# Kernel tuning notes

Measured on AMD Instinct MI355X. Metric: run time of the kernel, lower is better.

## Reference

```python
import jax, jax.numpy as jnp
import numpy as np

B, T, S, H, N = 4, 1024, 1024, 1024, 16
D = H // N
EPS = 1e-12
MASK_FILL = -1e6


def setup_inputs() -> dict:
    key = jax.random.key(0)
    ks = jax.random.split(key, 20)
    w = lambda i: jax.random.normal(ks[i], (H, H), jnp.float32) * 0.02
    zb = jnp.zeros((H,), jnp.float32)
    tgt_mask = jnp.tile(jnp.tril(jnp.ones((T, T), jnp.int32))[None], (B, 1, 1))
    return {
        "encoder_states": jax.random.normal(ks[0], (B, S, H), jnp.float32),
        "decoder_inputs": jax.random.normal(ks[1], (B, T, H), jnp.float32),
        "src_attn_mask": jnp.ones((B, S), jnp.int32),
        "tgt_attn_mask": tgt_mask,
        "q_w": w(2), "q_b": zb,
        "k_w": w(3), "k_b": zb,
        "v_w": w(4), "v_b": zb,
        "sq_w": w(5), "sq_b": zb,
        "sk_w": w(6), "sk_b": zb,
        "sv_w": w(7), "sv_b": zb,
        "dense_w": w(8), "dense_b": zb,
        "ln_g": jnp.ones((H,), jnp.float32),
        "ln_b": zb,
    }


def _layernorm(x, g, b):
    mu = jnp.mean(x, -1, keepdims=True)
    var = jnp.mean(jnp.square(x - mu), -1, keepdims=True)
    return (x - mu) * jax.lax.rsqrt(var + EPS) * g + b


def _attention(q, k, v, mask, dense_w, dense_b, ln_g, ln_b):
    # q:[B,Q,H] k,v:[B,K,H]; NOTE: original applies NO 1/sqrt(d) scaling.
    b, qlen, _ = q.shape
    klen = k.shape[1]
    qh = q.reshape(b, qlen, N, D).transpose(0, 2, 1, 3)  # [B,N,Q,D]
    kh = k.reshape(b, klen, N, D).transpose(0, 2, 1, 3)
    vh = v.reshape(b, klen, N, D).transpose(0, 2, 1, 3)
    scores = jnp.einsum('bnqd,bnkd->bnqk', qh, kh)
    m = mask.reshape(b, 1, qlen, klen) if mask.ndim == 3 else mask.reshape(b, 1, 1, klen)
    scores = jnp.where(m == 0, jnp.asarray(MASK_FILL, scores.dtype), scores)
    probs = jax.nn.softmax(scores, axis=-1)  # dropout = identity at eval
    ctx = jnp.einsum('bnqk,bnkd->bqnd', probs, vh)  # [B,Q,N,D]
    w = dense_w.T.reshape(N, D, H)
    proj = jnp.einsum('bqnd,ndh->bqh', ctx, w) + dense_b
    # Residual is q (the query projection), faithful to the original code.
    return _layernorm(q + proj, ln_g, ln_b)


def reference(encoder_states, decoder_inputs, src_attn_mask, tgt_attn_mask,
              q_w, q_b, k_w, k_b, v_w, v_b,
              sq_w, sq_b, sk_w, sk_b, sv_w, sv_b,
              dense_w, dense_b, ln_g, ln_b):
    lin = lambda x, w, b: x @ w.T + b
    # self-attention over decoder inputs
    q = lin(decoder_inputs, q_w, q_b)
    k = lin(decoder_inputs, k_w, k_b)
    v = lin(decoder_inputs, v_w, v_b)
    self_out = _attention(q, k, v, tgt_attn_mask, dense_w, dense_b, ln_g, ln_b)
    # cross-attention into encoder states (same dense/LayerNorm modules)
    q2 = lin(self_out, sq_w, sq_b)
    k2 = lin(encoder_states, sk_w, sk_b)
    v2 = lin(encoder_states, sv_w, sv_b)
    return _attention(q2, k2, v2, src_attn_mask, dense_w, dense_b, ln_g, ln_b)
```

## Files before the change

kernel.cpp:

```cpp
#include <hip/hip_runtime.h>

typedef __attribute__((ext_vector_type(4))) float f32x4;
typedef __attribute__((ext_vector_type(8))) short bf16x8;

#define GVOID const __attribute__((address_space(1))) void
#define LVOID __attribute__((address_space(3))) void

#define LOG2E 1.44269504f
#define LN2   0.69314718f

__device__ __forceinline__ float bf2f(ushort u){
  union { float f; unsigned int i; } c; c.i = ((unsigned int)u) << 16; return c.f;
}
__device__ __forceinline__ ushort f2bf(float f){
  union { float f; unsigned int i; } c; c.f = f;
  unsigned int r = (c.i + 0x7FFFu + ((c.i >> 16) & 1u)) >> 16;
  return (ushort)r;
}

struct CvtArgs {
  const float* s[9];
  ushort*      d[9];
  int          blks[9];
};
__global__ __launch_bounds__(256) void cvtk_multi(CvtArgs ca){
  int bid = blockIdx.x;
  int seg = 0, base = 0;
  while (bid - base >= ca.blks[seg]){ base += ca.blks[seg]; ++seg; }
  int i = ((bid - base) * 256 + threadIdx.x) * 4;
  float4 v = *(const float4*)(ca.s[seg] + i);
  ushort4 o;
  o.x = f2bf(v.x); o.y = f2bf(v.y); o.z = f2bf(v.z); o.w = f2bf(v.w);
  *(ushort4*)(ca.d[seg] + i) = o;
}

struct GemmArgs {
  const ushort* A[3];
  const ushort* W[3];
  const float*  bias[3];
  const ushort* R[3];
  ushort*       C[3];
  int           mode[3];
  float         scale[3];
};

__global__ __launch_bounds__(256,3) void gemm128(GemmArgs ga, int nmat, int N, int K){
  __shared__ ushort As[128 * 64];
  __shared__ ushort Bs[128 * 64];
  const int ntn = N >> 7;
  const int per = ntn * nmat;
  const int x = blockIdx.x & 7, ii = blockIdx.x >> 3;
  const int ipx = gridDim.x >> 3;
  const int gpx = ipx / per;
  const int tm = x * gpx + ii / per;
  const int q = ii % per;
  const int g = q / ntn, tn = q % ntn;
  const ushort* __restrict__ A = ga.A[g];
  const ushort* __restrict__ W = ga.W[g];
  const float*  __restrict__ bias = ga.bias[g];
  ushort* __restrict__ C = ga.C[g];
  const int mode = ga.mode[g];
  const float scale = ga.scale[g];

  const int t = threadIdx.x, lane = t & 63, wave = t >> 6;
  const int wr = wave >> 1, wc = wave & 1;
  const int l15 = lane & 15, l4 = lane >> 4;
  const int rowBase = tm * 128, colBase = tn * 128;

  f32x4 acc[4][4] = {};
  const int NT = K >> 6;
  for (int tk = 0; tk < NT; ++tk){
    const int k0 = tk * 64;
    __syncthreads();
#pragma unroll
    for (int j = 0; j < 4; ++j){
      int cb = j * 256 + wave * 64 + lane;
      int row = cb >> 3;
      int kc = (cb & 7) ^ (row & 7);
      const ushort* srcA = A + (size_t)(rowBase + row) * K + k0 + kc * 8;
      __builtin_amdgcn_global_load_lds((GVOID*)srcA, (LVOID*)(As + (size_t)cb * 8), 16, 0, 0);
      const ushort* srcB = W + (size_t)(colBase + row) * K + k0 + kc * 8;
      __builtin_amdgcn_global_load_lds((GVOID*)srcB, (LVOID*)(Bs + (size_t)cb * 8), 16, 0, 0);
    }
    __syncthreads();
#pragma unroll
    for (int kk = 0; kk < 2; ++kk){
      bf16x8 a[4], b[4];
#pragma unroll
      for (int m = 0; m < 4; ++m){
        int row = wr * 64 + m * 16 + l15;
        int ch = row * 8 + ((kk * 4 + l4) ^ (row & 7));
        a[m] = *(const bf16x8*)(As + ch * 8);
      }
#pragma unroll
      for (int n = 0; n < 4; ++n){
        int row = wc * 64 + n * 16 + l15;
        int ch = row * 8 + ((kk * 4 + l4) ^ (row & 7));
        b[n] = *(const bf16x8*)(Bs + ch * 8);
      }
#pragma unroll
      for (int m = 0; m < 4; ++m)
#pragma unroll
      for (int n = 0; n < 4; ++n)
        acc[m][n] = __builtin_amdgcn_mfma_f32_16x16x32_bf16(a[m], b[n], acc[m][n], 0, 0, 0);
    }
  }
#pragma unroll
  for (int m = 0; m < 4; ++m)
#pragma unroll
  for (int n = 0; n < 4; ++n)
#pragma unroll
  for (int r = 0; r < 4; ++r){
    int row = rowBase + wr * 64 + m * 16 + l4 * 4 + r;
    int col = colBase + wc * 64 + n * 16 + l15;
    float v = (acc[m][n][r] + bias[col]) * scale;
    if (mode == 2){
      int bb = row >> 10, tt = row & 1023, nh = col >> 6, d = col & 63;
      C[((size_t)((bb * 16 + nh) * 64 + d)) * 1024 + tt] = f2bf(v);
    } else {
      C[(size_t)row * N + col] = f2bf(v);
    }
  }
}

__global__ __launch_bounds__(256,3) void gemm_bt(GemmArgs ga, int nmat, int M, int N, int K){
  __shared__ ushort As[2][128 * 64];
  __shared__ ushort Bs[2][64 * 64];
  const int nb = gridDim.x;
  const int ntn = N >> 6;
  const int tq_cnt = ntn * nmat;
  const int x = blockIdx.x & 7, ii = blockIdx.x >> 3;
  const int ipx = nb >> 3;
  const int gpx = ipx / tq_cnt;
  const int tm = x * gpx + ii / tq_cnt;
  const int tq = ii % tq_cnt;
  const int g = tq / ntn, tn = tq % ntn;
  const ushort* __restrict__ A = ga.A[g];
  const ushort* __restrict__ W = ga.W[g];
  const float*  __restrict__ bias = ga.bias[g];
  const ushort* __restrict__ R = ga.R[g];
  ushort* __restrict__ C = ga.C[g];
  const int mode = ga.mode[g];
  const float scale = ga.scale[g];

  const int t = threadIdx.x, lane = t & 63, wave = t >> 6;
  const int wr = wave >> 1, wc = wave & 1;
  const int l15 = lane & 15, l4 = lane >> 4;
  const int rowBase = tm * 128, colBase = tn * 64;

  auto stage = [&](int buf, int k0){
#pragma unroll
    for (int j = 0; j < 4; ++j){
      int cb = j * 256 + wave * 64;
      int p = cb + lane;
      int row = p >> 3;
      int kc = (p & 7) ^ (row & 7);
      const ushort* src = A + (size_t)(rowBase + row) * K + k0 + kc * 8;
      __builtin_amdgcn_global_load_lds((GVOID*)src, (LVOID*)(&As[buf][cb * 8]), 16, 0, 0);
    }
#pragma unroll
    for (int j = 0; j < 2; ++j){
      int cb = j * 256 + wave * 64;
      int p = cb + lane;
      int row = p >> 3;
      int kc = (p & 7) ^ (row & 7);
      const ushort* src = W + (size_t)(colBase + row) * K + k0 + kc * 8;
      __builtin_amdgcn_global_load_lds((GVOID*)src, (LVOID*)(&Bs[buf][cb * 8]), 16, 0, 0);
    }
  };

  f32x4 acc[4][2] = {};
  const int NT = K >> 6;
  stage(0, 0);
  __syncthreads();
  for (int tk = 0; tk < NT; ++tk){
    const int cur = tk & 1;
    if (tk + 1 < NT) stage(cur ^ 1, (tk + 1) * 64);
#pragma unroll
    for (int kk = 0; kk < 2; ++kk){
      bf16x8 a[4], b[2];
#pragma unroll
      for (int m = 0; m < 4; ++m){
        int row = wr * 64 + m * 16 + l15;
        int ch = row * 8 + kk * 4 + l4;
        ch ^= (row & 7);
        a[m] = *(const bf16x8*)(&As[cur][ch * 8]);
      }
#pragma unroll
      for (int n = 0; n < 2; ++n){
        int row = wc * 32 + n * 16 + l15;
        int ch = row * 8 + kk * 4 + l4;
        ch ^= (row & 7);
        b[n] = *(const bf16x8*)(&Bs[cur][ch * 8]);
      }
#pragma unroll
      for (int m = 0; m < 4; ++m)
#pragma unroll
      for (int n = 0; n < 2; ++n)
        acc[m][n] = __builtin_amdgcn_mfma_f32_16x16x32_bf16(a[m], b[n], acc[m][n], 0, 0, 0);
    }
    __syncthreads();
  }
#pragma unroll
  for (int m = 0; m < 4; ++m)
#pragma unroll
  for (int n = 0; n < 2; ++n)
#pragma unroll
  for (int r = 0; r < 4; ++r){
    int row = rowBase + wr * 64 + m * 16 + l4 * 4 + r;
    int col = colBase + wc * 32 + n * 16 + l15;
    float v = (acc[m][n][r] + bias[col]) * scale;
    if (mode == 1) v += bf2f(R[(size_t)row * N + col]) * LN2;
    C[(size_t)row * N + col] = f2bf(v);
  }
}

__global__ __launch_bounds__(256,4) void attn_kernel(const ushort* __restrict__ Q, const ushort* __restrict__ Kv,
    const ushort* __restrict__ Vt, ushort* __restrict__ O, const int* __restrict__ smask, int causal){
  __shared__ ushort Ks[2][64 * 64];
  __shared__ ushort Vs[2][64 * 64];
  __shared__ __align__(16) char Ps[4][2048];
  const int p = blockIdx.x;
  const int x = p & 7, j = p >> 3;
  const int gg = x * 8 + (j & 7);
  const int b = gg >> 4, head = gg & 15;
  const int rr = j >> 3;
  int qt;
  if (causal){
    int lo = rr & 3, hi = rr >> 2;
    qt = (hi == 0) ? lo * 2 : (hi == 1) ? lo * 2 + 1 : (hi == 2) ? 15 - lo * 2 : 14 - lo * 2;
  } else qt = rr;
  const int t = threadIdx.x, lane = t & 63, wave = t >> 6;
  const int l15 = lane & 15, l4 = lane >> 4;
  const int qr0 = qt * 64 + wave * 16;
  const int sw = l15 << 3;

  bf16x8 aq[2];
#pragma unroll
  for (int kk = 0; kk < 2; ++kk)
    aq[kk] = *(const bf16x8*)(Q + (size_t)(b * 1024 + qr0 + l15) * 1024 + head * 64 + kk * 32 + l4 * 8);

  f32x4 cacc[4] = {};
  float mrow = -1e30f, lrow = 0.f;

  auto stage = [&](int buf, int k0){
#pragma unroll
    for (int jj = 0; jj < 2; ++jj){
      int cb = jj * 256 + wave * 64;
      int pp = cb + lane;
      int row = pp >> 3;
      int kc = (pp & 7) ^ (row & 7);
      const ushort* src = Kv + (size_t)(b * 1024 + k0 + row) * 1024 + head * 64 + kc * 8;
      __builtin_amdgcn_global_load_lds((GVOID*)src, (LVOID*)(&Ks[buf][cb * 8]), 16, 0, 0);
    }
#pragma unroll
    for (int jj = 0; jj < 2; ++jj){
      int cb = jj * 256 + wave * 64;
      int pp = cb + lane;
      int row = pp >> 3;
      int kc = (pp & 7) ^ (row & 7);
      const ushort* src = Vt + (size_t)((b * 16 + head) * 64 + row) * 1024 + k0 + kc * 8;
      __builtin_amdgcn_global_load_lds((GVOID*)src, (LVOID*)(&Vs[buf][cb * 8]), 16, 0, 0);
    }
  };

  const int nkt = causal ? (qt + 1) : 16;
  stage(0, 0);
  __syncthreads();
  char* Pb = &Ps[wave][0];
  for (int kt = 0; kt < nkt; ++kt){
    const int cur = kt & 1;
    const int k0 = kt * 64;
    if (kt + 1 < nkt) stage(cur ^ 1, (kt + 1) * 64);
    const ushort* Kb_ = &Ks[cur][0];
    const ushort* Vb_ = &Vs[cur][0];
    f32x4 st[4] = {};
#pragma unroll
    for (int kk = 0; kk < 2; ++kk){
      bf16x8 ak[4];
#pragma unroll
      for (int n = 0; n < 4; ++n){
        int row = n * 16 + l15;
        int ch = row * 8 + ((kk * 4 + l4) ^ (row & 7));
        ak[n] = *(const bf16x8*)(Kb_ + ch * 8);
      }
#pragma unroll
      for (int n = 0; n < 4; ++n)
        st[n] = __builtin_amdgcn_mfma_f32_16x16x32_bf16(ak[n], aq[kk], st[n], 0, 0, 0);
    }
    if (causal && k0 + 63 > qr0){
#pragma unroll
      for (int n = 0; n < 4; ++n)
#pragma unroll
      for (int r = 0; r < 4; ++r)
        if (k0 + n * 16 + l4 * 4 + r > qr0 + l15) st[n][r] = -1.5e6f;
    }
    if (smask){
      int myv = smask[b * 1024 + k0 + lane];
      if (!__all(myv != 0)){
#pragma unroll
        for (int n = 0; n < 4; ++n)
#pragma unroll
        for (int r = 0; r < 4; ++r){
          int mv = smask[b * 1024 + k0 + n * 16 + l4 * 4 + r];
          if (mv == 0) st[n][r] = -1.5e6f;
        }
      }
    }
    float mx = st[0][0];
#pragma unroll
    for (int n = 0; n < 4; ++n)
#pragma unroll
    for (int r = 0; r < 4; ++r) mx = fmaxf(mx, st[n][r]);
    mx = fmaxf(mx, __shfl_xor(mx, 16));
    mx = fmaxf(mx, __shfl_xor(mx, 32));
    if (!__all(mx <= mrow + 8.f)){
      float mn = fmaxf(mrow, mx);
      float scal = __builtin_amdgcn_exp2f(mrow - mn);
      mrow = mn;
      lrow *= scal;
#pragma unroll
      for (int r = 0; r < 4; ++r){
        float sb = __shfl(scal, l4 * 4 + r);
#pragma unroll
        for (int nd = 0; nd < 4; ++nd) cacc[nd][r] *= sb;
      }
    }
    float ps = 0.f;
#pragma unroll
    for (int n = 0; n < 4; ++n)
#pragma unroll
    for (int r = 0; r < 4; ++r){
      float pv = __builtin_amdgcn_exp2f(st[n][r] - mrow);
      st[n][r] = pv;
      ps += pv;
    }
    ps += __shfl_xor(ps, 16);
    ps += __shfl_xor(ps, 32);
    lrow += ps;
#pragma unroll
    for (int n = 0; n < 4; ++n){
      unsigned lo_, hi_;
      asm("v_cvt_pk_bf16_f32 %0, %1, %2" : "=v"(lo_) : "v"(st[n][0]), "v"(st[n][1]));
      asm("v_cvt_pk_bf16_f32 %0, %1, %2" : "=v"(hi_) : "v"(st[n][2]), "v"(st[n][3]));
      unsigned long long pk = (unsigned long long)lo_ | ((unsigned long long)hi_ << 32);
      *(unsigned long long*)(Pb + l15 * 128 + ((n * 32 + l4 * 8) ^ sw)) = pk;
    }
#pragma unroll
    for (int ks = 0; ks < 2; ++ks){
      bf16x8 bv[4];
#pragma unroll
      for (int nd = 0; nd < 4; ++nd){
        int row = nd * 16 + l15;
        int ch = row * 8 + ((ks * 4 + l4) ^ (row & 7));
        bv[nd] = *(const bf16x8*)(Vb_ + ch * 8);
      }
      int base = l15 * 128;
      int o = ks * 64 + l4 * 16;
      union { bf16x8 v; unsigned long long u[2]; } pa;
      pa.u[0] = *(const unsigned long long*)(Pb + base + ((o    ) ^ sw));
      pa.u[1] = *(const unsigned long long*)(Pb + base + ((o + 8) ^ sw));
#pragma unroll
      for (int nd = 0; nd < 4; ++nd)
        cacc[nd] = __builtin_amdgcn_mfma_f32_16x16x32_bf16(pa.v, bv[nd], cacc[nd], 0, 0, 0);
    }
    __syncthreads();
  }
#pragma unroll
  for (int r = 0; r < 4; ++r){
    float lb = __shfl(lrow, l4 * 4 + r);
    float inv = 1.f / lb;
    int row = qr0 + l4 * 4 + r;
#pragma unroll
    for (int nd = 0; nd < 4; ++nd){
      int col = head * 64 + nd * 16 + l15;
      O[(size_t)(b * 1024 + row) * 1024 + col] = f2bf(cacc[nd][r] * inv);
    }
  }
}

__global__ __launch_bounds__(256) void ln_kernel(const ushort* __restrict__ X, const float* __restrict__ g,
    const float* __restrict__ bta, ushort* __restrict__ outb, float* __restrict__ outf){
  const int row = blockIdx.x, t = threadIdx.x;
  const ushort* xr = X + (size_t)row * 1024;
  ushort4 u = *(const ushort4*)(xr + t * 4);
  float x0 = bf2f(u.x), x1 = bf2f(u.y), x2 = bf2f(u.z), x3 = bf2f(u.w);
  float s = x0 + x1 + x2 + x3;
  float s2 = x0 * x0 + x1 * x1 + x2 * x2 + x3 * x3;
#pragma unroll
  for (int d = 1; d < 64; d <<= 1){ s += __shfl_xor(s, d); s2 += __shfl_xor(s2, d); }
  __shared__ float red[8];
  const int lane = t & 63, wave = t >> 6;
  if (lane == 0){ red[wave] = s; red[4 + wave] = s2; }
  __syncthreads();
  s = red[0] + red[1] + red[2] + red[3];
  s2 = red[4] + red[5] + red[6] + red[7];
  float mu = s * (1.f / 1024.f);
  float var = fmaxf(s2 * (1.f / 1024.f) - mu * mu, 0.f);
  float rstd = rsqrtf(var + 1e-12f);
  int col = t * 4;
  float y0 = (x0 - mu) * rstd * g[col + 0] + bta[col + 0];
  float y1 = (x1 - mu) * rstd * g[col + 1] + bta[col + 1];
  float y2 = (x2 - mu) * rstd * g[col + 2] + bta[col + 2];
  float y3 = (x3 - mu) * rstd * g[col + 3] + bta[col + 3];
  if (outb){
    ushort4 o; o.x = f2bf(y0); o.y = f2bf(y1); o.z = f2bf(y2); o.w = f2bf(y3);
    *(ushort4*)(outb + (size_t)row * 1024 + col) = o;
  } else {
    float4 o; o.x = y0; o.y = y1; o.z = y2; o.w = y3;
    *(float4*)(outf + (size_t)row * 1024 + col) = o;
  }
}

extern "C" void kernel_launch(void* const* d_in, const int* in_sizes, int n_in,
                              void* d_out, int out_size, void* d_ws, size_t ws_size,
                              hipStream_t stream){
  const float* enc = (const float*)d_in[0];
  const float* dec = (const float*)d_in[1];
  const int* smask = (const int*)d_in[2];
  const float* q_w  = (const float*)d_in[4];  const float* q_b  = (const float*)d_in[5];
  const float* k_w  = (const float*)d_in[6];  const float* k_b  = (const float*)d_in[7];
  const float* v_w  = (const float*)d_in[8];  const float* v_b  = (const float*)d_in[9];
  const float* sq_w = (const float*)d_in[10]; const float* sq_b = (const float*)d_in[11];
  const float* sk_w = (const float*)d_in[12]; const float* sk_b = (const float*)d_in[13];
  const float* sv_w = (const float*)d_in[14]; const float* sv_b = (const float*)d_in[15];
  const float* dw   = (const float*)d_in[16]; const float* db   = (const float*)d_in[17];
  const float* lng  = (const float*)d_in[18]; const float* lnb  = (const float*)d_in[19];
  ushort* ws = (ushort*)d_ws;
  const size_t MEG = 1024u * 1024u;
  ushort* decb = ws + 0 * MEG;
  ushort* encb = ws + 4 * MEG;
  ushort* Qb   = ws + 8 * MEG;
  ushort* Kb   = ws + 12 * MEG;
  ushort* Vtb  = ws + 20 * MEG;
  ushort* ctx  = ws + 24 * MEG;
  ushort* S1   = ws + 28 * MEG;
  ushort* Wq  = ws + 32 * MEG; ushort* Wk  = ws + 33 * MEG; ushort* Wv  = ws + 34 * MEG;
  ushort* Wsq = ws + 35 * MEG; ushort* Wsk = ws + 36 * MEG; ushort* Wsv = ws + 37 * MEG;
  ushort* Wd  = ws + 38 * MEG;
  const int M = 4096, N = 1024, Kd = 1024;
  {
    CvtArgs ca;
    ca.s[0] = dec;  ca.d[0] = decb; ca.blks[0] = 4096;
    ca.s[1] = enc;  ca.d[1] = encb; ca.blks[1] = 4096;
    ca.s[2] = q_w;  ca.d[2] = Wq;   ca.blks[2] = 1024;
    ca.s[3] = k_w;  ca.d[3] = Wk;   ca.blks[3] = 1024;
    ca.s[4] = v_w;  ca.d[4] = Wv;   ca.blks[4] = 1024;
    ca.s[5] = sq_w; ca.d[5] = Wsq;  ca.blks[5] = 1024;
    ca.s[6] = sk_w; ca.d[6] = Wsk;  ca.blks[6] = 1024;
    ca.s[7] = sv_w; ca.d[7] = Wsv;  ca.blks[7] = 1024;
    ca.s[8] = dw;   ca.d[8] = Wd;   ca.blks[8] = 1024;
    cvtk_multi<<<15360, 256, 0, stream>>>(ca);
  }
  {
    GemmArgs ga = {};
    ga.A[0] = decb; ga.A[1] = decb; ga.A[2] = decb;
    ga.W[0] = Wq;   ga.W[1] = Wk;   ga.W[2] = Wv;
    ga.bias[0] = q_b; ga.bias[1] = k_b; ga.bias[2] = v_b;
    ga.C[0] = Qb;   ga.C[1] = Kb;   ga.C[2] = Vtb;
    ga.mode[0] = 0; ga.mode[1] = 0; ga.mode[2] = 2;
    ga.scale[0] = LOG2E; ga.scale[1] = 1.f; ga.scale[2] = 1.f;
    gemm128<<<768, 256, 0, stream>>>(ga, 3, N, Kd);
  }
  attn_kernel<<<1024, 256, 0, stream>>>(Qb, Kb, Vtb, ctx, nullptr, 1);
  {
    GemmArgs ga = {};
    ga.A[0] = ctx; ga.W[0] = Wd; ga.bias[0] = db; ga.R[0] = Qb; ga.C[0] = S1; ga.mode[0] = 1;
    ga.scale[0] = 1.f;
    gemm_bt<<<512, 256, 0, stream>>>(ga, 1, M, N, Kd);
  }
  ln_kernel<<<4096, 256, 0, stream>>>(S1, lng, lnb, decb, nullptr);
  {
    GemmArgs ga = {};
    ga.A[0] = decb; ga.A[1] = encb; ga.A[2] = encb;
    ga.W[0] = Wsq;  ga.W[1] = Wsk;  ga.W[2] = Wsv;
    ga.bias[0] = sq_b; ga.bias[1] = sk_b; ga.bias[2] = sv_b;
    ga.C[0] = Qb;   ga.C[1] = Kb;   ga.C[2] = Vtb;
    ga.mode[0] = 0; ga.mode[1] = 0; ga.mode[2] = 2;
    ga.scale[0] = LOG2E; ga.scale[1] = 1.f; ga.scale[2] = 1.f;
    gemm128<<<768, 256, 0, stream>>>(ga, 3, N, Kd);
  }
  attn_kernel<<<1024, 256, 0, stream>>>(Qb, Kb, Vtb, ctx, smask, 0);
  {
    GemmArgs ga = {};
    ga.A[0] = ctx; ga.W[0] = Wd; ga.bias[0] = db; ga.R[0] = Qb; ga.C[0] = S1; ga.mode[0] = 1;
    ga.scale[0] = 1.f;
    gemm_bt<<<512, 256, 0, stream>>>(ga, 1, M, N, Kd);
  }
  ln_kernel<<<4096, 256, 0, stream>>>(S1, lng, lnb, nullptr, (float*)d_out);
}
```

Measured before the change: 205.4 us.

## Shrink QKV GEMM row tile and stage attention K/V through registers

The QKV projection GEMM drops from 128x128 to 64x128 tiles. It launches twice as many blocks with higher occupancy bounds, and the bias load is hoisted out of the epilogue's inner loop. The attention kernel drops its double-buffered global_load_lds staging. It now prefetches the next K/V tile into registers during compute and writes it to a single LDS buffer after a barrier. This halves attention LDS use but adds an extra sync per tile, and the smaller GEMM tiles lower data reuse.

```diff
diff --git a/kernel.cpp b/kernel.cpp
--- a/kernel.cpp
+++ b/kernel.cpp
@@ -44,8 +44,8 @@
   float         scale[3];
 };
 
-__global__ __launch_bounds__(256,3) void gemm128(GemmArgs ga, int nmat, int N, int K){
-  __shared__ ushort As[128 * 64];
+__global__ __launch_bounds__(256,6) void gemmqkv(GemmArgs ga, int nmat, int N, int K){
+  __shared__ ushort As[64 * 64];
   __shared__ ushort Bs[128 * 64];
   const int ntn = N >> 7;
   const int per = ntn * nmat;
@@ -65,30 +65,36 @@
   const int t = threadIdx.x, lane = t & 63, wave = t >> 6;
   const int wr = wave >> 1, wc = wave & 1;
   const int l15 = lane & 15, l4 = lane >> 4;
-  const int rowBase = tm * 128, colBase = tn * 128;
-
-  f32x4 acc[4][4] = {};
+  const int rowBase = tm * 64, colBase = tn * 128;
+
+  f32x4 acc[2][4] = {};
   const int NT = K >> 6;
   for (int tk = 0; tk < NT; ++tk){
     const int k0 = tk * 64;
     __syncthreads();
 #pragma unroll
-    for (int j = 0; j < 4; ++j){
-      int cb = j * 256 + wave * 64 + lane;
+    for (int j = 0; j < 2; ++j){
+      int cb = j * 256 + t;
       int row = cb >> 3;
       int kc = (cb & 7) ^ (row & 7);
       const ushort* srcA = A + (size_t)(rowBase + row) * K + k0 + kc * 8;
       __builtin_amdgcn_global_load_lds((GVOID*)srcA, (LVOID*)(As + (size_t)cb * 8), 16, 0, 0);
+    }
+#pragma unroll
+    for (int j = 0; j < 4; ++j){
+      int cb = j * 256 + t;
+      int row = cb >> 3;
+      int kc = (cb & 7) ^ (row & 7);
       const ushort* srcB = W + (size_t)(colBase + row) * K + k0 + kc * 8;
       __builtin_amdgcn_global_load_lds((GVOID*)srcB, (LVOID*)(Bs + (size_t)cb * 8), 16, 0, 0);
     }
     __syncthreads();
 #pragma unroll
     for (int kk = 0; kk < 2; ++kk){
-      bf16x8 a[4], b[4];
-#pragma unroll
-      for (int m = 0; m < 4; ++m){
-        int row = wr * 64 + m * 16 + l15;
+      bf16x8 a[2], b[4];
+#pragma unroll
+      for (int m = 0; m < 2; ++m){
+        int row = wr * 32 + m * 16 + l15;
         int ch = row * 8 + ((kk * 4 + l4) ^ (row & 7));
         a[m] = *(const bf16x8*)(As + ch * 8);
       }
@@ -99,26 +105,28 @@
         b[n] = *(const bf16x8*)(Bs + ch * 8);
       }
 #pragma unroll
-      for (int m = 0; m < 4; ++m)
+      for (int m = 0; m < 2; ++m)
 #pragma unroll
       for (int n = 0; n < 4; ++n)
         acc[m][n] = __builtin_amdgcn_mfma_f32_16x16x32_bf16(a[m], b[n], acc[m][n], 0, 0, 0);
     }
   }
 #pragma unroll
-  for (int m = 0; m < 4; ++m)
-#pragma unroll
-  for (int n = 0; n < 4; ++n)
-#pragma unroll
-  for (int r = 0; r < 4; ++r){
-    int row = rowBase + wr * 64 + m * 16 + l4 * 4 + r;
+  for (int m = 0; m < 2; ++m)
+#pragma unroll
+  for (int n = 0; n < 4; ++n){
     int col = colBase + wc * 64 + n * 16 + l15;
-    float v = (acc[m][n][r] + bias[col]) * scale;
-    if (mode == 2){
-      int bb = row >> 10, tt = row & 1023, nh = col >> 6, d = col & 63;
-      C[((size_t)((bb * 16 + nh) * 64 + d)) * 1024 + tt] = f2bf(v);
-    } else {
-      C[(size_t)row * N + col] = f2bf(v);
+    float bi = bias[col];
+#pragma unroll
+    for (int r = 0; r < 4; ++r){
+      int row = rowBase + wr * 32 + m * 16 + l4 * 4 + r;
+      float v = (acc[m][n][r] + bi) * scale;
+      if (mode == 2){
+        int bb = row >> 10, tt = row & 1023, nh = col >> 6, d = col & 63;
+        C[((size_t)((bb * 16 + nh) * 64 + d)) * 1024 + tt] = f2bf(v);
+      } else {
+        C[(size_t)row * N + col] = f2bf(v);
+      }
     }
   }
 }
@@ -217,8 +225,8 @@
 
 __global__ __launch_bounds__(256,4) void attn_kernel(const ushort* __restrict__ Q, const ushort* __restrict__ Kv,
     const ushort* __restrict__ Vt, ushort* __restrict__ O, const int* __restrict__ smask, int causal){
-  __shared__ ushort Ks[2][64 * 64];
-  __shared__ ushort Vs[2][64 * 64];
+  __shared__ ushort Ks[64 * 64];
+  __shared__ ushort Vs[64 * 64];
   __shared__ __align__(16) char Ps[4][2048];
   const int p = blockIdx.x;
   const int x = p & 7, j = p >> 3;
@@ -243,37 +251,38 @@
   f32x4 cacc[4] = {};
   float mrow = -1e30f, lrow = 0.f;
 
-  auto stage = [&](int buf, int k0){
+  uint4 kreg[2], vreg[2];
+  int srow[2], skc[2];
+#pragma unroll
+  for (int jj = 0; jj < 2; ++jj){
+    int pp = jj * 256 + wave * 64 + lane;
+    srow[jj] = pp >> 3;
+    skc[jj] = (pp & 7) ^ (srow[jj] & 7);
+  }
+  auto loadRegs = [&](int k0){
 #pragma unroll
     for (int jj = 0; jj < 2; ++jj){
-      int cb = jj * 256 + wave * 64;
-      int pp = cb + lane;
-      int row = pp >> 3;
-      int kc = (pp & 7) ^ (row & 7);
-      const ushort* src = Kv + (size_t)(b * 1024 + k0 + row) * 1024 + head * 64 + kc * 8;
-      __builtin_amdgcn_global_load_lds((GVOID*)src, (LVOID*)(&Ks[buf][cb * 8]), 16, 0, 0);
-    }
+      kreg[jj] = *(const uint4*)(Kv + (size_t)(b * 1024 + k0 + srow[jj]) * 1024 + head * 64 + skc[jj] * 8);
+      vreg[jj] = *(const uint4*)(Vt + (size_t)((b * 16 + head) * 64 + srow[jj]) * 1024 + k0 + skc[jj] * 8);
+    }
+  };
+  auto writeLDS = [&](){
 #pragma unroll
     for (int jj = 0; jj < 2; ++jj){
-      int cb = jj * 256 + wave * 64;
-      int pp = cb + lane;
-      int row = pp >> 3;
-      int kc = (pp & 7) ^ (row & 7);
-      const ushort* src = Vt + (size_t)((b * 16 + head) * 64 + row) * 1024 + k0 + kc * 8;
-      __builtin_amdgcn_global_load_lds((GVOID*)src, (LVOID*)(&Vs[buf][cb * 8]), 16, 0, 0);
+      int pp = jj * 256 + wave * 64 + lane;
+      *(uint4*)(Ks + (size_t)pp * 8) = kreg[jj];
+      *(uint4*)(Vs + (size_t)pp * 8) = vreg[jj];
     }
   };
 
   const int nkt = causal ? (qt + 1) : 16;
-  stage(0, 0);
+  loadRegs(0);
+  writeLDS();
   __syncthreads();
   char* Pb = &Ps[wave][0];
   for (int kt = 0; kt < nkt; ++kt){
-    const int cur = kt & 1;
     const int k0 = kt * 64;
-    if (kt + 1 < nkt) stage(cur ^ 1, (kt + 1) * 64);
-    const ushort* Kb_ = &Ks[cur][0];
-    const ushort* Vb_ = &Vs[cur][0];
+    if (kt + 1 < nkt) loadRegs((kt + 1) * 64);
     f32x4 st[4] = {};
 #pragma unroll
     for (int kk = 0; kk < 2; ++kk){
@@ -282,7 +291,7 @@
       for (int n = 0; n < 4; ++n){
         int row = n * 16 + l15;
         int ch = row * 8 + ((kk * 4 + l4) ^ (row & 7));
-        ak[n] = *(const bf16x8*)(Kb_ + ch * 8);
+        ak[n] = *(const bf16x8*)(Ks + ch * 8);
       }
 #pragma unroll
       for (int n = 0; n < 4; ++n)
@@ -353,7 +362,7 @@
       for (int nd = 0; nd < 4; ++nd){
         int row = nd * 16 + l15;
         int ch = row * 8 + ((ks * 4 + l4) ^ (row & 7));
-        bv[nd] = *(const bf16x8*)(Vb_ + ch * 8);
+        bv[nd] = *(const bf16x8*)(Vs + ch * 8);
       }
       int base = l15 * 128;
       int o = ks * 64 + l4 * 16;
@@ -365,6 +374,10 @@
         cacc[nd] = __builtin_amdgcn_mfma_f32_16x16x32_bf16(pa.v, bv[nd], cacc[nd], 0, 0, 0);
     }
     __syncthreads();
+    if (kt + 1 < nkt){
+      writeLDS();
+      __syncthreads();
+    }
   }
 #pragma unroll
   for (int r = 0; r < 4; ++r){
@@ -460,7 +473,7 @@
     ga.C[0] = Qb;   ga.C[1] = Kb;   ga.C[2] = Vtb;
     ga.mode[0] = 0; ga.mode[1] = 0; ga.mode[2] = 2;
     ga.scale[0] = LOG2E; ga.scale[1] = 1.f; ga.scale[2] = 1.f;
-    gemm128<<<768, 256, 0, stream>>>(ga, 3, N, Kd);
+    gemmqkv<<<1536, 256, 0, stream>>>(ga, 3, N, Kd);
   }
   attn_kernel<<<1024, 256, 0, stream>>>(Qb, Kb, Vtb, ctx, nullptr, 1);
   {
@@ -478,7 +491,7 @@
     ga.C[0] = Qb;   ga.C[1] = Kb;   ga.C[2] = Vtb;
     ga.mode[0] = 0; ga.mode[1] = 0; ga.mode[2] = 2;
     ga.scale[0] = LOG2E; ga.scale[1] = 1.f; ga.scale[2] = 1.f;
-    gemm128<<<768, 256, 0, stream>>>(ga, 3, N, Kd);
+    gemmqkv<<<1536, 256, 0, stream>>>(ga, 3, N, Kd);
   }
   attn_kernel<<<1024, 256, 0, stream>>>(Qb, Kb, Vtb, ctx, smask, 0);
   {
```

New measurement: 290.6 us. 41.5% more time.
